# Performance work log

Measured on AMD Instinct MI355X. Metric: run time of the kernel, lower is better.

## Reference

```python
import math
import jax, jax.numpy as jnp
import numpy as np

DMODEL = 512
NUM_HEADS = 8
HEAD_DIM = DMODEL // NUM_HEADS
MAX_LEN = 1024
L = 2 * MAX_LEN - 1  # 2047
B = 4
S = 1024  # src_len == max_len


def setup_inputs() -> dict:
    key = jax.random.key(0)
    ks = jax.random.split(key, 12)
    f32 = jnp.float32
    inp = {
        "query": jax.random.normal(ks[0], (B, S, DMODEL), f32),
        "key": jax.random.normal(ks[1], (B, S, DMODEL), f32),
        "value": jax.random.normal(ks[2], (B, S, DMODEL), f32),
        # nn.Linear weights (y = x @ W.T + b)
        "Wq": jax.random.normal(ks[3], (DMODEL, DMODEL), f32) * 0.02,
        "bq": jnp.zeros((DMODEL,), f32),
        "Wk": jax.random.normal(ks[4], (DMODEL, DMODEL), f32) * 0.02,
        "bk": jnp.zeros((DMODEL,), f32),
        "Wv": jax.random.normal(ks[5], (DMODEL, DMODEL), f32) * 0.02,
        "bv": jnp.zeros((DMODEL,), f32),
        # relative position tables (torch.randn init)
        "quaver_Er": jax.random.normal(ks[6], (NUM_HEADS, L, HEAD_DIM), f32),
        "beat_Er": jax.random.normal(ks[7], (NUM_HEADS, L // 4, HEAD_DIM), f32),
        "bar_Er": jax.random.normal(ks[8], (NUM_HEADS, L // 16, HEAD_DIM), f32),
    }
    return inp


def _skew(QEr):
    # QEr: [b, h, S, 2S-1] -> [b, h, S, S] via pad-reshape-slice trick
    b, h, s, l = QEr.shape
    x = jnp.pad(QEr, ((0, 0), (0, 0), (0, 0), (0, 1)))        # [b,h,S,2S]
    x = x.reshape(b, h, -1)                                    # [b,h,S*2S]
    x = jnp.pad(x, ((0, 0), (0, 0), (0, l - s)))               # [b,h,(S+1)*(2S-1)]
    x = x.reshape(b, h, s + 1, l)
    return x[:, :, :s, -s:]


def _skew_chunked(QEr, rep):
    # Faithful to skew_beat/skew_bar: repeat_interleave(rep) along last dim, then
    # roll each chunk of `rep` rows (chunk i) by i*rep, then take last S cols.
    b, h, s, lr = QEr.shape
    x = jnp.repeat(QEr, rep, axis=-1)                          # [b,h,S,rep*lr]
    w = rep * lr
    shifts = (jnp.arange(s) // rep) * rep                      # [S]
    # torch.roll: out[c] = in[(c - shift) mod W]
    cols = (jnp.arange(w)[None, :] - shifts[:, None]) % w      # [S, W]
    x = jnp.take_along_axis(x, cols[None, None], axis=-1)
    return x[:, :, :s, -s:]


def reference(query, key, value, Wq, bq, Wk, bk, Wv, bv, quaver_Er, beat_Er, bar_Er):
    bs, src_len, d_model = query.shape
    h, hd = NUM_HEADS, HEAD_DIM
    max_len = MAX_LEN

    q = (query @ Wq.T + bq).reshape(bs, src_len, h, hd).transpose(0, 2, 1, 3)   # [b,h,S,d]
    k = (key @ Wk.T + bk).reshape(bs, src_len, h, hd).transpose(0, 2, 3, 1)      # [b,h,d,S]
    v = (value @ Wv.T + bv).reshape(bs, src_len, h, hd).transpose(0, 2, 1, 3)    # [b,h,S,d]

    Er_q = quaver_Er[:, max_len - src_len:max_len + src_len, :]                  # [h,2S-1,d]
    Er_b = beat_Er[:, (max_len - src_len) // 4:(max_len + src_len) // 4, :]      # [h,~S/2,d]
    Er_r = bar_Er[:, (max_len - src_len) // 16:(max_len + src_len) // 16, :]     # [h,~S/8,d]

    QEr_q = jnp.einsum('bhsd,hld->bhsl', q, Er_q)
    QEr_b = jnp.einsum('bhsd,hld->bhsl', q, Er_b)
    QEr_r = jnp.einsum('bhsd,hld->bhsl', q, Er_r)

    Srel = _skew(QEr_q)
    Srel_beat = _skew_chunked(QEr_b, 4)
    Srel_bar = _skew_chunked(QEr_r, 16)

    attn = (jnp.matmul(q, k) + Srel + Srel_beat + Srel_bar) / math.sqrt(hd)
    attn = jax.nn.softmax(attn, axis=-1)
    out = jnp.matmul(attn, v)                                                    # [b,h,S,d]
    out = out.transpose(0, 2, 1, 3).reshape(bs, src_len, d_model)
    return out, attn
```

## Files before the change

kernel.cpp:

```cpp
#include <hip/hip_runtime.h>


typedef float f32x4 __attribute__((ext_vector_type(4)));
typedef short s16x8 __attribute__((ext_vector_type(8)));
typedef short s16x4 __attribute__((ext_vector_type(4)));
typedef __bf16 bf16x8 __attribute__((ext_vector_type(8)));

static __device__ __forceinline__ short f2bf(float f) {
    return __builtin_bit_cast(short, (__bf16)f);
}
static __device__ __forceinline__ float bf2f(short s) {
    union { unsigned u; float f; } v;
    v.u = ((unsigned)(unsigned short)s) << 16;
    return v.f;
}
static __device__ __forceinline__ f32x4 MM(s16x8 a, s16x8 b, f32x4 c) {
    return __builtin_amdgcn_mfma_f32_16x16x32_bf16(
        __builtin_bit_cast(bf16x8, a), __builtin_bit_cast(bf16x8, b), c, 0, 0, 0);
}
#define KEEP(x) asm volatile("" : "+v"(x))

struct CvtArgs {
    const float* src[9];
    short* dst[9];
    unsigned n[9];
};

__global__ __launch_bounds__(256) void convert_kernel(CvtArgs a) {
    const int ai = blockIdx.y;
    const unsigned n = a.n[ai];
    const float* __restrict__ s = a.src[ai];
    short* __restrict__ d = a.dst[ai];
    const unsigned stride = gridDim.x * 256 * 8;
    for (unsigned base = (blockIdx.x * 256 + threadIdx.x) * 8; base < n; base += stride) {
        f32x4 v0 = *(const f32x4*)(s + base);
        f32x4 v1 = *(const f32x4*)(s + base + 4);
        s16x8 o;
        o[0] = f2bf(v0[0]); o[1] = f2bf(v0[1]); o[2] = f2bf(v0[2]); o[3] = f2bf(v0[3]);
        o[4] = f2bf(v1[0]); o[5] = f2bf(v1[1]); o[6] = f2bf(v1[2]); o[7] = f2bf(v1[3]);
        *(s16x8*)(d + base) = o;
    }
}

__global__ __launch_bounds__(128, 2) void proj_kernel(
    const short* __restrict__ queryb, const short* __restrict__ keyb, const short* __restrict__ valueb,
    const short* __restrict__ Wqb, const float* __restrict__ bq,
    const short* __restrict__ Wkb, const float* __restrict__ bk,
    const short* __restrict__ Wvb, const float* __restrict__ bv,
    short* __restrict__ qb, short* __restrict__ kb, short* __restrict__ vT)
{
    const int tid = threadIdx.x;
    const int wid = tid >> 6, lane = tid & 63;
    const int l15 = lane & 15, grp = lane >> 4;
    const int gid = blockIdx.x * 2 + wid;
    const int z = gid >> 9;
    const int r = gid & 511;

    const short *Am, *Bm;
    const float* bias;
    int a0, b0;
    if (z == 0)      { Am = Wqb;    Bm = queryb; bias = bq; a0 = (r >> 6) * 64; b0 = (r & 63) * 64; }
    else if (z == 1) { Am = Wkb;    Bm = keyb;   bias = bk; a0 = (r >> 6) * 64; b0 = (r & 63) * 64; }
    else             { Am = valueb; Bm = Wvb;    bias = bv; a0 = (r >> 3) * 64; b0 = (r & 7) * 64; }

    f32x4 acc[4][4];
    #pragma unroll
    for (int i = 0; i < 4; ++i)
        #pragma unroll
        for (int j = 0; j < 4; ++j)
            acc[i][j] = f32x4{0.f, 0.f, 0.f, 0.f};

    const short* arow0 = Am + (size_t)(a0 + l15) * 512 + grp * 8;
    const short* brow0 = Bm + (size_t)(b0 + l15) * 512 + grp * 8;

    s16x8 aA[4], bA[4], aB[4], bB[4];
    #pragma unroll
    for (int i = 0; i < 4; ++i) {
        aA[i] = *(const s16x8*)(arow0 + (size_t)i * 16 * 512);
        bA[i] = *(const s16x8*)(brow0 + (size_t)i * 16 * 512);
    }
    for (int kk = 0; kk < 512; kk += 32) {
        const int kn = kk + 32;
        if (kn < 512) {
            #pragma unroll
            for (int i = 0; i < 4; ++i) {
                aB[i] = *(const s16x8*)(arow0 + (size_t)i * 16 * 512 + kn);
                bB[i] = *(const s16x8*)(brow0 + (size_t)i * 16 * 512 + kn);
            }
        }
        #pragma unroll
        for (int i = 0; i < 4; ++i)
            #pragma unroll
            for (int j = 0; j < 4; ++j)
                acc[i][j] = MM(aA[i], bA[j], acc[i][j]);
        #pragma unroll
        for (int i = 0; i < 4; ++i) { aA[i] = aB[i]; bA[i] = bB[i]; }
    }

    if (z < 2) {
        short* dst = (z == 0) ? qb : kb;
        #pragma unroll
        for (int i = 0; i < 4; ++i) {
            const int f0 = a0 + i * 16 + grp * 4;
            const f32x4 bv4 = *(const f32x4*)&bias[f0];
            const int h = f0 >> 6, d0 = f0 & 63;
            #pragma unroll
            for (int j = 0; j < 4; ++j) {
                const int srow = b0 + j * 16 + l15;
                const int bb = srow >> 10, sl = srow & 1023;
                s16x4 o;
                #pragma unroll
                for (int g = 0; g < 4; ++g)
                    o[g] = f2bf(acc[i][j][g] + bv4[g]);
                *(s16x4*)&dst[(size_t)((bb * 8 + h) * 1024 + sl) * 64 + d0] = o;
            }
        }
    } else {
        #pragma unroll
        for (int j = 0; j < 4; ++j) {
            const int n = b0 + j * 16 + l15;
            const float bval = bias[n];
            const int h = n >> 6, d = n & 63;
            #pragma unroll
            for (int i = 0; i < 4; ++i) {
                const int s0 = a0 + i * 16 + grp * 4;
                const int bb = s0 >> 10, sl = s0 & 1023;
                s16x4 o;
                #pragma unroll
                for (int g = 0; g < 4; ++g)
                    o[g] = f2bf(acc[i][j][g] + bval);
                *(s16x4*)&vT[(size_t)((bb * 8 + h) * 64 + d) * 1024 + sl] = o;
            }
        }
    }
}

__global__ __launch_bounds__(512, 2) void attn_kernel(
    const short* __restrict__ Eqb, const short* __restrict__ Ebb, const short* __restrict__ Errb,
    const short* __restrict__ qb, const short* __restrict__ kb, const short* __restrict__ vT,
    float* __restrict__ out, float* __restrict__ attn)
{
    __shared__ __align__(16) char smem[155008];
    short* PS   = (short*)(smem + 86784);
    float* PACC = (float*)(smem + 119680);

    const int tid = threadIdx.x;
    const int wid = tid >> 6, lane = tid & 63;
    const int l15 = lane & 15, grp = lane >> 4;

    const int orig = blockIdx.x;
    const int bid = (orig & 7) * 32 + (orig >> 3);

    const int bh = bid >> 3;
    const int chunk = bid & 7;
    const int h = bh & 7;
    const int b = bh >> 3;

    const short* EqH = Eqb  + (size_t)h * 2047 * 64;
    const short* EbH = Ebb  + (size_t)h * 511 * 64;
    const short* ErH = Errb + (size_t)h * 127 * 64;
    const short* qbH = qb + (size_t)bh * 1024 * 64;
    const short* kbH = kb + (size_t)bh * 1024 * 64;
    const short* vTH = vT + (size_t)bh * 64 * 1024;

    auto buildT = [&](int i0s, int bb01, s16x8 q0, s16x8 q1) {
        short* RQ2 = (short*)(smem + bb01 * 32896);
        short* RB2 = (short*)(smem + 65792 + bb01 * 8320);
        short* RR2 = (short*)(smem + 82432 + bb01 * 2176);
        const int qbase = 1008 - i0s;
        for (int cs = wid; cs < 65; cs += 8) {
            const int c = cs * 16 + l15;
            int erow = qbase + c; if (erow > 2046) erow = 2046;
            const short* ep = EqH + (size_t)erow * 64 + grp * 8;
            s16x8 e0 = *(const s16x8*)ep;
            s16x8 e1 = *(const s16x8*)(ep + 32);
            f32x4 a = f32x4{0.f, 0.f, 0.f, 0.f};
            a = MM(q0, e0, a);
            a = MM(q1, e1, a);
            #pragma unroll
            for (int g = 0; g < 4; ++g) {
                const int ii = grp * 4 + g;
                const int j = c - 15 + ii;
                if (j >= 0 && j < 1024) RQ2[ii * 1028 + j] = f2bf(a[g]);
            }
        }
        const int bbase = 252 - (i0s >> 2);
        for (int cs = wid; cs < 17; cs += 8) {
            const int c = cs * 16 + l15;
            int erow = bbase + c; if (erow > 510) erow = 510;
            const short* ep = EbH + (size_t)erow * 64 + grp * 8;
            s16x8 e0 = *(const s16x8*)ep;
            s16x8 e1 = *(const s16x8*)(ep + 32);
            f32x4 a = f32x4{0.f, 0.f, 0.f, 0.f};
            a = MM(q0, e0, a);
            a = MM(q1, e1, a);
            const int jq = c - 3 + grp;
            if (jq >= 0 && jq < 256) {
                #pragma unroll
                for (int g = 0; g < 4; ++g)
                    RB2[(grp * 4 + g) * 260 + jq] = f2bf(a[g]);
            }
        }
        const int rbase = 63 - (i0s >> 4);
        if (wid < 4) {
            const int c = wid * 16 + l15;
            const short* ep = ErH + (size_t)(rbase + c) * 64 + grp * 8;
            s16x8 e0 = *(const s16x8*)ep;
            s16x8 e1 = *(const s16x8*)(ep + 32);
            f32x4 a = f32x4{0.f, 0.f, 0.f, 0.f};
            a = MM(q0, e0, a);
            a = MM(q1, e1, a);
            #pragma unroll
            for (int g = 0; g < 4; ++g)
                RR2[(grp * 4 + g) * 68 + c] = f2bf(a[g]);
        }
    };

    const int i00 = chunk * 128;
    s16x8 qA0 = *(const s16x8*)(qbH + (size_t)(i00 + l15) * 64 + grp * 8);
    s16x8 qA1 = *(const s16x8*)(qbH + (size_t)(i00 + l15) * 64 + 32 + grp * 8);

    s16x8 kf[8][2];
    #pragma unroll
    for (int t = 0; t < 8; ++t) {
        const short* kp = kbH + (size_t)(wid * 128 + t * 16 + l15) * 64 + grp * 8;
        kf[t][0] = *(const s16x8*)kp;
        kf[t][1] = *(const s16x8*)(kp + 32);
    }
    s16x8 vreg[16];
    #pragma unroll
    for (int dvt = 0; dvt < 4; ++dvt)
        #pragma unroll
        for (int kc = 0; kc < 4; ++kc)
            vreg[dvt * 4 + kc] = *(const s16x8*)(vTH + (size_t)(dvt * 16 + l15) * 1024
                                                 + wid * 128 + kc * 32 + grp * 8);

    buildT(i00, 0, qA0, qA1);
    __syncthreads();

    const float SC = 0.125f * 1.4426950408889634f;
    const int swz = (l15 & 3) << 5;

    for (int s = 0; s < 8; ++s) {
        #pragma unroll
        for (int t = 0; t < 8; ++t) { KEEP(kf[t][0]); KEEP(kf[t][1]); }
        #pragma unroll
        for (int z = 0; z < 16; ++z) KEEP(vreg[z]);

        const int cur = s & 1;
        const int i0 = chunk * 128 + s * 16;
        short* RQ2c = (short*)(smem + cur * 32896);
        short* RB2c = (short*)(smem + 65792 + cur * 8320);
        short* RR2c = (short*)(smem + 82432 + cur * 2176);
        float* RSUMc = (float*)(smem + 154496 + cur * 256);

        s16x8 qn0, qn1;
        if (s < 7) {
            qn0 = *(const s16x8*)(qbH + (size_t)(i0 + 16 + l15) * 64 + grp * 8);
            qn1 = *(const s16x8*)(qbH + (size_t)(i0 + 16 + l15) * 64 + 32 + grp * 8);
        }

        f32x4 p[8];
        #pragma unroll
        for (int t = 0; t < 8; ++t) {
            f32x4 a = f32x4{0.f, 0.f, 0.f, 0.f};
            a = MM(kf[t][0], qA0, a);
            a = MM(kf[t][1], qA1, a);
            const int jb2 = wid * 128 + t * 16 + grp * 4;
            s16x4 gq4 = *(const s16x4*)&RQ2c[l15 * 1028 + jb2];
            const float rb = bf2f(RB2c[l15 * 260 + wid * 32 + t * 4 + grp]);
            const float rr = bf2f(RR2c[l15 * 68 + wid * 8 + t]);
            const float add = rb + rr;
            f32x4 pe;
            #pragma unroll
            for (int g = 0; g < 4; ++g)
                pe[g] = exp2f((a[g] + bf2f(gq4[g]) + add) * SC);
            p[t] = pe;
        }

        float part = 0.f;
        #pragma unroll
        for (int t = 0; t < 8; ++t)
            #pragma unroll
            for (int g = 0; g < 4; ++g)
                part += p[t][g];
        part += __shfl_xor(part, 16, 64);
        part += __shfl_xor(part, 32, 64);
        if (lane < 16) RSUMc[lane * 8 + wid] = part;

        #pragma unroll
        for (int t = 0; t < 8; ++t) {
            const int col = (wid * 128 + t * 16 + grp * 4) ^ swz;
            s16x4 o;
            #pragma unroll
            for (int g = 0; g < 4; ++g) o[g] = f2bf(p[t][g]);
            *(s16x4*)&PS[l15 * 1028 + col] = o;
        }
        __syncthreads();

        float rinv;
        {
            f32x4 s0 = *(const f32x4*)&RSUMc[l15 * 8];
            f32x4 s1 = *(const f32x4*)&RSUMc[l15 * 8 + 4];
            rinv = 1.0f / (s0[0] + s0[1] + s0[2] + s0[3] + s1[0] + s1[1] + s1[2] + s1[3]);
        }

        if (s < 7) buildT(i0 + 16, cur ^ 1, qn0, qn1);

        f32x4 acc[4];
        #pragma unroll
        for (int dvt = 0; dvt < 4; ++dvt) acc[dvt] = f32x4{0.f, 0.f, 0.f, 0.f};
        #pragma unroll
        for (int kc = 0; kc < 4; ++kc) {
            const int col = (wid * 128 + kc * 32 + grp * 8) ^ swz;
            s16x8 bfrag = *(const s16x8*)&PS[l15 * 1028 + col];
            #pragma unroll
            for (int dvt = 0; dvt < 4; ++dvt)
                acc[dvt] = MM(vreg[dvt * 4 + kc], bfrag, acc[dvt]);
        }
        #pragma unroll
        for (int dvt = 0; dvt < 4; ++dvt)
            *(f32x4*)&PACC[(wid * 16 + l15) * 68 + dvt * 16 + grp * 4] = acc[dvt];
        __syncthreads();

        if (tid < 256) {
            const int i = tid >> 4, dvq = tid & 15;
            f32x4 o = f32x4{0.f, 0.f, 0.f, 0.f};
            #pragma unroll
            for (int w = 0; w < 8; ++w)
                o += *(const f32x4*)&PACC[(w * 16 + i) * 68 + dvq * 4];
            f32x4 s0 = *(const f32x4*)&RSUMc[i * 8];
            f32x4 s1 = *(const f32x4*)&RSUMc[i * 8 + 4];
            const float ri = 1.0f / (s0[0] + s0[1] + s0[2] + s0[3] + s1[0] + s1[1] + s1[2] + s1[3]);
            o *= ri;
            *(f32x4*)&out[(size_t)(b * 1024 + i0 + i) * 512 + h * 64 + dvq * 4] = o;
        }

        {
            float* arow = attn + (size_t)(bh * 1024 + i0 + l15) * 1024;
            #pragma unroll
            for (int t = 0; t < 8; ++t) {
                f32x4 o = p[t] * rinv;
                *(f32x4*)&arow[wid * 128 + t * 16 + grp * 4] = o;
            }
        }

        if (s < 7) { qA0 = qn0; qA1 = qn1; }
    }
}

extern "C" void kernel_launch(void* const* d_in, const int* in_sizes, int n_in,
                              void* d_out, int out_size, void* d_ws, size_t ws_size,
                              hipStream_t stream)
{
    const float* query = (const float*)d_in[0];
    const float* key   = (const float*)d_in[1];
    const float* value = (const float*)d_in[2];
    const float* Wq = (const float*)d_in[3];
    const float* bq = (const float*)d_in[4];
    const float* Wk = (const float*)d_in[5];
    const float* bk = (const float*)d_in[6];
    const float* Wv = (const float*)d_in[7];
    const float* bv = (const float*)d_in[8];
    const float* Eq = (const float*)d_in[9];
    const float* Eb = (const float*)d_in[10];
    const float* Er = (const float*)d_in[11];

    float* out  = (float*)d_out;
    float* attn = out + (size_t)4 * 1024 * 512;

    short* qb     = (short*)d_ws;
    short* kb     = qb     + 2097152;
    short* vT     = kb     + 2097152;
    short* queryb = vT     + 2097152;
    short* keyb   = queryb + 2097152;
    short* valueb = keyb   + 2097152;
    short* Wqb    = valueb + 2097152;
    short* Wkb    = Wqb    + 262144;
    short* Wvb    = Wkb    + 262144;
    short* Eqb    = Wvb    + 262144;
    short* Ebb    = Eqb    + 1048064;
    short* Errb   = Ebb    + 261632;

    CvtArgs a;
    a.src[0] = query; a.dst[0] = queryb; a.n[0] = 2097152;
    a.src[1] = key;   a.dst[1] = keyb;   a.n[1] = 2097152;
    a.src[2] = value; a.dst[2] = valueb; a.n[2] = 2097152;
    a.src[3] = Wq;    a.dst[3] = Wqb;    a.n[3] = 262144;
    a.src[4] = Wk;    a.dst[4] = Wkb;    a.n[4] = 262144;
    a.src[5] = Wv;    a.dst[5] = Wvb;    a.n[5] = 262144;
    a.src[6] = Eq;    a.dst[6] = Eqb;    a.n[6] = 1048064;
    a.src[7] = Eb;    a.dst[7] = Ebb;    a.n[7] = 261632;
    a.src[8] = Er;    a.dst[8] = Errb;   a.n[8] = 65024;

    convert_kernel<<<dim3(1024, 9), 256, 0, stream>>>(a);
    proj_kernel<<<768, 128, 0, stream>>>(queryb, keyb, valueb,
                                         Wqb, bq, Wkb, bk, Wvb, bv, qb, kb, vT);
    attn_kernel<<<256, 512, 0, stream>>>(Eqb, Ebb, Errb, qb, kb, vT, out, attn);
}
```

Baseline: 129.5 us.

## Software-pipeline Er loads, use LDS-only barriers, fast exp2, reorder attn stores

The relative-position table builds now prefetch Er rows two or three iterations ahead, so global load latency overlaps the MFMA work. Full __syncthreads are replaced by barriers that only wait on LDS/scalar counters, so outstanding global stores no longer stall each barrier. exp2f becomes the hardware exp2 builtin, and the attn-probability global stores move ahead of the PV MFMAs so they overlap compute. The convert kernel grid also shrinks from 1024 to 64 blocks per array. The prefetch reads past the loop end (clamped rows) and uses more registers; the barrier relies on the assumption that global writes need no ordering across the block.

```diff
diff --git a/kernel.cpp b/kernel.cpp
--- a/kernel.cpp
+++ b/kernel.cpp
@@ -19,6 +19,7 @@
         __builtin_bit_cast(bf16x8, a), __builtin_bit_cast(bf16x8, b), c, 0, 0, 0);
 }
 #define KEEP(x) asm volatile("" : "+v"(x))
+#define BARL() asm volatile("s_waitcnt lgkmcnt(0)\n\ts_barrier" ::: "memory")
 
 struct CvtArgs {
     const float* src[9];
@@ -168,37 +169,56 @@
         short* RB2 = (short*)(smem + 65792 + bb01 * 8320);
         short* RR2 = (short*)(smem + 82432 + bb01 * 2176);
         const int qbase = 1008 - i0s;
-        for (int cs = wid; cs < 65; cs += 8) {
-            const int c = cs * 16 + l15;
-            int erow = qbase + c; if (erow > 2046) erow = 2046;
-            const short* ep = EqH + (size_t)erow * 64 + grp * 8;
-            s16x8 e0 = *(const s16x8*)ep;
-            s16x8 e1 = *(const s16x8*)(ep + 32);
-            f32x4 a = f32x4{0.f, 0.f, 0.f, 0.f};
-            a = MM(q0, e0, a);
-            a = MM(q1, e1, a);
-            #pragma unroll
-            for (int g = 0; g < 4; ++g) {
-                const int ii = grp * 4 + g;
-                const int j = c - 15 + ii;
-                if (j >= 0 && j < 1024) RQ2[ii * 1028 + j] = f2bf(a[g]);
+        {
+            auto ldq = [&](int cs, s16x8& e0, s16x8& e1) {
+                int erow = qbase + cs * 16 + l15; if (erow > 2046) erow = 2046;
+                const short* ep = EqH + (size_t)erow * 64 + grp * 8;
+                e0 = *(const s16x8*)ep;
+                e1 = *(const s16x8*)(ep + 32);
+            };
+            s16x8 A0, A1, B0, B1, C0, C1;
+            ldq(wid, A0, A1);
+            ldq(wid + 8, B0, B1);
+            ldq(wid + 16, C0, C1);
+            for (int cs = wid; cs < 65; cs += 8) {
+                f32x4 a = f32x4{0.f, 0.f, 0.f, 0.f};
+                a = MM(q0, A0, a);
+                a = MM(q1, A1, a);
+                A0 = B0; A1 = B1; B0 = C0; B1 = C1;
+                ldq(cs + 24, C0, C1);
+                const int c = cs * 16 + l15;
+                #pragma unroll
+                for (int g = 0; g < 4; ++g) {
+                    const int ii = grp * 4 + g;
+                    const int j = c - 15 + ii;
+                    if (j >= 0 && j < 1024) RQ2[ii * 1028 + j] = f2bf(a[g]);
+                }
             }
         }
         const int bbase = 252 - (i0s >> 2);
-        for (int cs = wid; cs < 17; cs += 8) {
-            const int c = cs * 16 + l15;
-            int erow = bbase + c; if (erow > 510) erow = 510;
-            const short* ep = EbH + (size_t)erow * 64 + grp * 8;
-            s16x8 e0 = *(const s16x8*)ep;
-            s16x8 e1 = *(const s16x8*)(ep + 32);
-            f32x4 a = f32x4{0.f, 0.f, 0.f, 0.f};
-            a = MM(q0, e0, a);
-            a = MM(q1, e1, a);
-            const int jq = c - 3 + grp;
-            if (jq >= 0 && jq < 256) {
-                #pragma unroll
-                for (int g = 0; g < 4; ++g)
-                    RB2[(grp * 4 + g) * 260 + jq] = f2bf(a[g]);
+        {
+            auto ldb = [&](int cs, s16x8& e0, s16x8& e1) {
+                int erow = bbase + cs * 16 + l15; if (erow > 510) erow = 510;
+                const short* ep = EbH + (size_t)erow * 64 + grp * 8;
+                e0 = *(const s16x8*)ep;
+                e1 = *(const s16x8*)(ep + 32);
+            };
+            s16x8 A0, A1, B0, B1;
+            ldb(wid, A0, A1);
+            ldb(wid + 8, B0, B1);
+            for (int cs = wid; cs < 17; cs += 8) {
+                f32x4 a = f32x4{0.f, 0.f, 0.f, 0.f};
+                a = MM(q0, A0, a);
+                a = MM(q1, A1, a);
+                A0 = B0; A1 = B1;
+                ldb(cs + 16, B0, B1);
+                const int c = cs * 16 + l15;
+                const int jq = c - 3 + grp;
+                if (jq >= 0 && jq < 256) {
+                    #pragma unroll
+                    for (int g = 0; g < 4; ++g)
+                        RB2[(grp * 4 + g) * 260 + jq] = f2bf(a[g]);
+                }
             }
         }
         const int rbase = 63 - (i0s >> 4);
@@ -236,7 +256,7 @@
                                                  + wid * 128 + kc * 32 + grp * 8);
 
     buildT(i00, 0, qA0, qA1);
-    __syncthreads();
+    BARL();
 
     const float SC = 0.125f * 1.4426950408889634f;
     const int swz = (l15 & 3) << 5;
@@ -274,7 +294,7 @@
             f32x4 pe;
             #pragma unroll
             for (int g = 0; g < 4; ++g)
-                pe[g] = exp2f((a[g] + bf2f(gq4[g]) + add) * SC);
+                pe[g] = __builtin_amdgcn_exp2f((a[g] + bf2f(gq4[g]) + add) * SC);
             p[t] = pe;
         }
 
@@ -296,7 +316,7 @@
             for (int g = 0; g < 4; ++g) o[g] = f2bf(p[t][g]);
             *(s16x4*)&PS[l15 * 1028 + col] = o;
         }
-        __syncthreads();
+        BARL();
 
         float rinv;
         {
@@ -307,6 +327,16 @@
 
         if (s < 7) buildT(i0 + 16, cur ^ 1, qn0, qn1);
 
+        {
+            float* arow = attn + (size_t)(bh * 1024 + i0 + l15) * 1024;
+            #pragma unroll
+            for (int t = 0; t < 8; ++t) {
+                f32x4 o = p[t] * rinv;
+                *(f32x4*)&arow[wid * 128 + t * 16 + grp * 4] = o;
+            }
+        }
+
+        const int kh = wid & 1;  (void)kh;
         f32x4 acc[4];
         #pragma unroll
         for (int dvt = 0; dvt < 4; ++dvt) acc[dvt] = f32x4{0.f, 0.f, 0.f, 0.f};
@@ -321,7 +351,7 @@
         #pragma unroll
         for (int dvt = 0; dvt < 4; ++dvt)
             *(f32x4*)&PACC[(wid * 16 + l15) * 68 + dvt * 16 + grp * 4] = acc[dvt];
-        __syncthreads();
+        BARL();
 
         if (tid < 256) {
             const int i = tid >> 4, dvq = tid & 15;
@@ -334,15 +364,6 @@
             const float ri = 1.0f / (s0[0] + s0[1] + s0[2] + s0[3] + s1[0] + s1[1] + s1[2] + s1[3]);
             o *= ri;
             *(f32x4*)&out[(size_t)(b * 1024 + i0 + i) * 512 + h * 64 + dvq * 4] = o;
-        }
-
-        {
-            float* arow = attn + (size_t)(bh * 1024 + i0 + l15) * 1024;
-            #pragma unroll
-            for (int t = 0; t < 8; ++t) {
-                f32x4 o = p[t] * rinv;
-                *(f32x4*)&arow[wid * 128 + t * 16 + grp * 4] = o;
-            }
         }
 
         if (s < 7) { qA0 = qn0; qA1 = qn1; }
@@ -393,7 +414,7 @@
     a.src[7] = Eb;    a.dst[7] = Ebb;    a.n[7] = 261632;
     a.src[8] = Er;    a.dst[8] = Errb;   a.n[8] = 65024;
 
-    convert_kernel<<<dim3(1024, 9), 256, 0, stream>>>(a);
+    convert_kernel<<<dim3(64, 9), 256, 0, stream>>>(a);
     proj_kernel<<<768, 128, 0, stream>>>(queryb, keyb, valueb,
                                          Wqb, bq, Wkb, bk, Wvb, bv, qb, kb, vT);
     attn_kernel<<<256, 512, 0, stream>>>(Eqb, Ebb, Errb, qb, kb, vT, out, attn);
```

Result: slower. 139.7 us (+7.9%).
